# Optimization experiments

Measured on AMD Instinct MI355X. Metric: run time of the kernel, lower is better.

## Reference

```python
import jax, jax.numpy as jnp
import numpy as np

PARTIAL_DATA_THRESHOLD = 0.1  # threshold on squared NN distance (ChamferDistance returns squared dists)


def setup_inputs() -> dict:
    key = jax.random.key(0)
    k1, k2 = jax.random.split(key)
    scan_vertices = jax.random.normal(k1, (50000, 3), dtype=jnp.float32)      # N x 3
    template_vertices = jax.random.normal(k2, (6890, 3), dtype=jnp.float32)   # M x 3
    return {"scan_vertices": scan_vertices, "template_vertices": template_vertices}


def reference(scan_vertices, template_vertices):
    # Directional (template -> scan) Chamfer: for each template point, squared
    # distance to nearest scan point; then sum distances below threshold.
    # d2[m, n] = |t_m|^2 + |s_n|^2 - 2 t_m . s_n
    t_sq = jnp.sum(template_vertices * template_vertices, axis=-1)            # [M]
    s_sq = jnp.sum(scan_vertices * scan_vertices, axis=-1)                    # [N]
    cross = jnp.einsum('md,nd->mn', template_vertices, scan_vertices)         # [M, N]
    d2 = t_sq[:, None] + s_sq[None, :] - 2.0 * cross                          # [M, N]
    template2scan = jnp.min(d2, axis=1)                                       # [M]
    mask = template2scan < PARTIAL_DATA_THRESHOLD
    return jnp.sum(jnp.where(mask, template2scan, 0.0))
```

## Files before the change

### kernel.cpp

```cpp
#include <hip/hip_runtime.h>
#include <hip/hip_bf16.h>

#define BLK 256
#define SPLITS 44
#define FRTOT 1584
#define FPS (FRTOT / SPLITS)
#define NSLOT (FRTOT * 32)
#define THRESH 0.1f
#define KEY_MAX 0xFFFFFFFFu
#define ONE_BF ((unsigned short)0x3F80)

typedef __attribute__((ext_vector_type(8))) short short8;
typedef __attribute__((ext_vector_type(16))) float floatx16;

__device__ __forceinline__ unsigned short f2bf(float x) {
    unsigned u = __float_as_uint(x);
    unsigned r = u + 0x7FFFu + ((u >> 16) & 1u);
    return (unsigned short)(r >> 16);
}
__device__ __forceinline__ float bf2f(unsigned short h) {
    return __uint_as_float(((unsigned)h) << 16);
}

__device__ __forceinline__ unsigned f2key(float f) {
    unsigned b = __float_as_uint(f);
    return (b & 0x80000000u) ? ~b : (b | 0x80000000u);
}
__device__ __forceinline__ float key2f(unsigned k) {
    return __uint_as_float((k & 0x80000000u) ? (k & 0x7FFFFFFFu) : ~k);
}

template <int CTRL>
__device__ __forceinline__ float dpp_ror_min(float v) {
    const int i = __float_as_int(v);
    const int p = __builtin_amdgcn_update_dpp(i, i, CTRL, 0xF, 0xF, false);
    return fminf(v, __int_as_float(p));
}

__global__ __launch_bounds__(BLK) void pdl_prep(const float* __restrict__ scan,
                                                uint4* __restrict__ fragbuf,
                                                unsigned* __restrict__ gmin,
                                                float* __restrict__ out,
                                                int N, int Mpad) {
    const int n = blockIdx.x * BLK + threadIdx.x;
    if (n == 0) out[0] = 0.0f;
    if (n < Mpad) gmin[n] = KEY_MAX;
    if (n >= NSLOT) return;

    unsigned short k[16];
    if (n < N) {
        const float x = scan[3 * n + 0], y = scan[3 * n + 1], z = scan[3 * n + 2];
        const float s2 = fmaf(x, x, fmaf(y, y, z * z));
        const float cx = -2.0f * x, cy = -2.0f * y, cz = -2.0f * z;
        const unsigned short xh = f2bf(cx); const unsigned short xl = f2bf(cx - bf2f(xh));
        const unsigned short yh = f2bf(cy); const unsigned short yl = f2bf(cy - bf2f(yh));
        const unsigned short zh = f2bf(cz); const unsigned short zl = f2bf(cz - bf2f(zh));
        const unsigned short wh = f2bf(s2); const unsigned short wl = f2bf(s2 - bf2f(wh));
        k[0] = xh; k[1] = xl; k[2] = xh; k[3] = xl;
        k[4] = yh; k[5] = yl; k[6] = yh; k[7] = yl;
        k[8] = zh; k[9] = zl; k[10] = zh; k[11] = zl;
        k[12] = ONE_BF; k[13] = ONE_BF;
        k[14] = wh; k[15] = wl;
    } else {
#pragma unroll
        for (int i = 0; i < 16; ++i) k[i] = 0;
        k[12] = ONE_BF; k[13] = ONE_BF;
        k[14] = f2bf(1e30f); k[15] = 0;
    }

    const int g = n >> 5, c = n & 31;
    uint4 lo, hi;
    lo.x = (unsigned)k[0] | ((unsigned)k[1] << 16);
    lo.y = (unsigned)k[2] | ((unsigned)k[3] << 16);
    lo.z = (unsigned)k[4] | ((unsigned)k[5] << 16);
    lo.w = (unsigned)k[6] | ((unsigned)k[7] << 16);
    hi.x = (unsigned)k[8] | ((unsigned)k[9] << 16);
    hi.y = (unsigned)k[10] | ((unsigned)k[11] << 16);
    hi.z = (unsigned)k[12] | ((unsigned)k[13] << 16);
    hi.w = (unsigned)k[14] | ((unsigned)k[15] << 16);
    fragbuf[(size_t)g * 64 + c] = lo;
    fragbuf[(size_t)g * 64 + 32 + c] = hi;
}

__device__ __forceinline__ short8 make_A(const float* __restrict__ tmpl, int m, bool hi) {
    const float x = tmpl[3 * m + 0], y = tmpl[3 * m + 1], z = tmpl[3 * m + 2];
    const float t2 = fmaf(x, x, fmaf(y, y, z * z));
    const unsigned short xh = f2bf(x); const unsigned short xl = f2bf(x - bf2f(xh));
    const unsigned short yh = f2bf(y); const unsigned short yl = f2bf(y - bf2f(yh));
    const unsigned short zh = f2bf(z); const unsigned short zl = f2bf(z - bf2f(zh));
    const unsigned short wh = f2bf(t2); const unsigned short wl = f2bf(t2 - bf2f(wh));
    short8 A;
    A[0] = (short)(hi ? zh : xh);
    A[1] = (short)(hi ? zh : xh);
    A[2] = (short)(hi ? zl : xl);
    A[3] = (short)(hi ? zl : xl);
    A[4] = (short)(hi ? wh : yh);
    A[5] = (short)(hi ? wl : yh);
    A[6] = (short)(hi ? ONE_BF : yl);
    A[7] = (short)(hi ? ONE_BF : yl);
    return A;
}

__device__ __forceinline__ void reduce_store(floatx16 mn, int mbase, int lane,
                                             unsigned* __restrict__ gmin) {
#pragma unroll
    for (int r = 0; r < 16; ++r) {
        float v = mn[r];
        v = dpp_ror_min<0x128>(v);
        v = dpp_ror_min<0x124>(v);
        v = dpp_ror_min<0x122>(v);
        v = dpp_ror_min<0x121>(v);
        const int sw = __builtin_amdgcn_ds_swizzle(__float_as_int(v), 0x401F);
        v = fminf(v, __int_as_float(sw));
        if ((lane & 31) == 0) {
            const int row = (r & 3) + 8 * (r >> 2) + ((lane >> 5) << 2);
            atomicMin(&gmin[mbase + row], f2key(v));
        }
    }
}

__global__ __launch_bounds__(BLK, 4) void pdl_main(const float* __restrict__ tmpl,
                                                   const uint4* __restrict__ fragbuf,
                                                   unsigned* __restrict__ gmin,
                                                   int M) {
    const int tid = threadIdx.x;
    const int wave = tid >> 6, lane = tid & 63;
    const bool hi = (lane >= 32);

    const int mbase = (blockIdx.y * 4 + wave) * 64;
    int m0 = mbase + (lane & 31);       if (m0 > M - 1) m0 = M - 1;
    int m1 = mbase + 32 + (lane & 31);  if (m1 > M - 1) m1 = M - 1;
    const short8 A0 = make_A(tmpl, m0, hi);
    const short8 A1 = make_A(tmpl, m1, hi);

    floatx16 mn0, mn1, zacc;
#pragma unroll
    for (int r = 0; r < 16; ++r) { mn0[r] = 3e30f; mn1[r] = 3e30f; zacc[r] = 0.0f; }

    const uint4* fb = fragbuf + (size_t)(blockIdx.x * FPS) * 64 + lane;

    union U { uint4 u; short8 s; };
    uint4 p0 = fb[0];
    uint4 p1 = fb[64];
#pragma unroll 1
    for (int f = 0; f < FPS; f += 2) {
        U c0, c1; c0.u = p0; c1.u = p1;
        p0 = fb[(size_t)(f + 2) * 64];
        p1 = fb[(size_t)(f + 3) * 64];
        const floatx16 d00 = __builtin_amdgcn_mfma_f32_32x32x16_bf16(A0, c0.s, zacc, 0, 0, 0);
        const floatx16 d01 = __builtin_amdgcn_mfma_f32_32x32x16_bf16(A0, c1.s, zacc, 0, 0, 0);
#pragma unroll
        for (int r = 0; r < 16; ++r)
            mn0[r] = fminf(fminf(d00[r], d01[r]), mn0[r]);
        const floatx16 d10 = __builtin_amdgcn_mfma_f32_32x32x16_bf16(A1, c0.s, zacc, 0, 0, 0);
        const floatx16 d11 = __builtin_amdgcn_mfma_f32_32x32x16_bf16(A1, c1.s, zacc, 0, 0, 0);
#pragma unroll
        for (int r = 0; r < 16; ++r)
            mn1[r] = fminf(fminf(d10[r], d11[r]), mn1[r]);
    }

    reduce_store(mn0, mbase, lane, gmin);
    reduce_store(mn1, mbase + 32, lane, gmin);
}

__global__ __launch_bounds__(BLK) void pdl_final(const unsigned* __restrict__ gmin,
                                                 float* __restrict__ out, int M) {
    const int m = blockIdx.x * BLK + threadIdx.x;
    float s = 0.0f;
    if (m < M) {
        const float v = key2f(gmin[m]);
        if (v < THRESH) s = v;
    }
#pragma unroll
    for (int off = 32; off > 0; off >>= 1) s += __shfl_down(s, off, 64);

    __shared__ float ls[BLK / 64];
    const int lane = threadIdx.x & 63;
    const int w = threadIdx.x >> 6;
    if (lane == 0) ls[w] = s;
    __syncthreads();
    if (threadIdx.x == 0) {
        float t = 0.0f;
#pragma unroll
        for (int i = 0; i < BLK / 64; ++i) t += ls[i];
        atomicAdd(out, t);
    }
}

extern "C" void kernel_launch(void* const* d_in, const int* in_sizes, int n_in,
                              void* d_out, int out_size, void* d_ws, size_t ws_size,
                              hipStream_t stream) {
    const float* scan = (const float*)d_in[0];
    const float* tmpl = (const float*)d_in[1];
    float* out = (float*)d_out;

    const int N = in_sizes[0] / 3;
    const int M = in_sizes[1] / 3;

    const int tGroups = (M + 255) / 256;
    const int Mpad = ((M + 31) / 32) * 32 + 128;

    unsigned* gmin = (unsigned*)d_ws;
    uint4* fragbuf = (uint4*)((char*)d_ws + 65536);

    pdl_prep<<<(NSLOT + BLK - 1) / BLK, BLK, 0, stream>>>(scan, fragbuf, gmin,
                                                          out, N, Mpad);

    dim3 grid(SPLITS, tGroups);
    pdl_main<<<grid, BLK, 0, stream>>>(tmpl, fragbuf, gmin, M);

    pdl_final<<<(M + BLK - 1) / BLK, BLK, 0, stream>>>(gmin, out, M);
}
```

Measured before the change: 88.74 us.

## Give each wave four template tiles and split scan fragments across waves

The block's four waves now share one 128-row template block, and each wave walks a quarter of the block's scan-fragment range. Each scan fragment loaded is therefore reused across four template tiles instead of two. SPLITS is halved and the tGroups grid dimension doubles, so the total block count stays roughly the same. The change raises register pressure (four accumulator tiles, launch bounds lowered to 3) and doubles the atomicMin traffic per template row, because four waves now write the same rows.

```diff
diff --git a/kernel.cpp b/kernel.cpp
--- a/kernel.cpp
+++ b/kernel.cpp
@@ -2,9 +2,10 @@
 #include <hip/hip_bf16.h>
 
 #define BLK 256
-#define SPLITS 44
+#define SPLITS 22
 #define FRTOT 1584
 #define FPS (FRTOT / SPLITS)
+#define WFRAGS (FPS / 4)
 #define NSLOT (FRTOT * 32)
 #define THRESH 0.1f
 #define KEY_MAX 0xFFFFFFFFu
@@ -119,7 +120,7 @@
     }
 }
 
-__global__ __launch_bounds__(BLK, 4) void pdl_main(const float* __restrict__ tmpl,
+__global__ __launch_bounds__(BLK, 3) void pdl_main(const float* __restrict__ tmpl,
                                                    const uint4* __restrict__ fragbuf,
                                                    unsigned* __restrict__ gmin,
                                                    int M) {
@@ -127,40 +128,55 @@
     const int wave = tid >> 6, lane = tid & 63;
     const bool hi = (lane >= 32);
 
-    const int mbase = (blockIdx.y * 4 + wave) * 64;
-    int m0 = mbase + (lane & 31);       if (m0 > M - 1) m0 = M - 1;
-    int m1 = mbase + 32 + (lane & 31);  if (m1 > M - 1) m1 = M - 1;
+    const int mbase = blockIdx.y * 128;
+    int m0 = mbase + (lane & 31);        if (m0 > M - 1) m0 = M - 1;
+    int m1 = mbase + 32 + (lane & 31);   if (m1 > M - 1) m1 = M - 1;
+    int m2 = mbase + 64 + (lane & 31);   if (m2 > M - 1) m2 = M - 1;
+    int m3 = mbase + 96 + (lane & 31);   if (m3 > M - 1) m3 = M - 1;
     const short8 A0 = make_A(tmpl, m0, hi);
     const short8 A1 = make_A(tmpl, m1, hi);
-
-    floatx16 mn0, mn1, zacc;
-#pragma unroll
-    for (int r = 0; r < 16; ++r) { mn0[r] = 3e30f; mn1[r] = 3e30f; zacc[r] = 0.0f; }
-
-    const uint4* fb = fragbuf + (size_t)(blockIdx.x * FPS) * 64 + lane;
+    const short8 A2 = make_A(tmpl, m2, hi);
+    const short8 A3 = make_A(tmpl, m3, hi);
+
+    floatx16 mn0, mn1, mn2, mn3, zacc;
+#pragma unroll
+    for (int r = 0; r < 16; ++r) {
+        mn0[r] = 3e30f; mn1[r] = 3e30f; mn2[r] = 3e30f; mn3[r] = 3e30f;
+        zacc[r] = 0.0f;
+    }
+
+    const uint4* fb = fragbuf +
+        (size_t)(blockIdx.x * FPS + wave * WFRAGS) * 64 + lane;
 
     union U { uint4 u; short8 s; };
     uint4 p0 = fb[0];
     uint4 p1 = fb[64];
 #pragma unroll 1
-    for (int f = 0; f < FPS; f += 2) {
+    for (int f = 0; f < WFRAGS; f += 2) {
         U c0, c1; c0.u = p0; c1.u = p1;
         p0 = fb[(size_t)(f + 2) * 64];
         p1 = fb[(size_t)(f + 3) * 64];
-        const floatx16 d00 = __builtin_amdgcn_mfma_f32_32x32x16_bf16(A0, c0.s, zacc, 0, 0, 0);
-        const floatx16 d01 = __builtin_amdgcn_mfma_f32_32x32x16_bf16(A0, c1.s, zacc, 0, 0, 0);
-#pragma unroll
-        for (int r = 0; r < 16; ++r)
-            mn0[r] = fminf(fminf(d00[r], d01[r]), mn0[r]);
-        const floatx16 d10 = __builtin_amdgcn_mfma_f32_32x32x16_bf16(A1, c0.s, zacc, 0, 0, 0);
-        const floatx16 d11 = __builtin_amdgcn_mfma_f32_32x32x16_bf16(A1, c1.s, zacc, 0, 0, 0);
-#pragma unroll
-        for (int r = 0; r < 16; ++r)
-            mn1[r] = fminf(fminf(d10[r], d11[r]), mn1[r]);
+#define PDL_STEP(Af, mnf)                                                          \
+        {                                                                          \
+            const floatx16 d0 =                                                    \
+                __builtin_amdgcn_mfma_f32_32x32x16_bf16(Af, c0.s, zacc, 0, 0, 0);  \
+            const floatx16 d1 =                                                    \
+                __builtin_amdgcn_mfma_f32_32x32x16_bf16(Af, c1.s, zacc, 0, 0, 0);  \
+            _Pragma("unroll")                                                      \
+            for (int r = 0; r < 16; ++r)                                           \
+                mnf[r] = fminf(fminf(d0[r], d1[r]), mnf[r]);                       \
+        }
+        PDL_STEP(A0, mn0)
+        PDL_STEP(A1, mn1)
+        PDL_STEP(A2, mn2)
+        PDL_STEP(A3, mn3)
+#undef PDL_STEP
     }
 
     reduce_store(mn0, mbase, lane, gmin);
     reduce_store(mn1, mbase + 32, lane, gmin);
+    reduce_store(mn2, mbase + 64, lane, gmin);
+    reduce_store(mn3, mbase + 96, lane, gmin);
 }
 
 __global__ __launch_bounds__(BLK) void pdl_final(const unsigned* __restrict__ gmin,
@@ -197,7 +213,7 @@
     const int N = in_sizes[0] / 3;
     const int M = in_sizes[1] / 3;
 
-    const int tGroups = (M + 255) / 256;
+    const int tGroups = (M + 127) / 128;
     const int Mpad = ((M + 31) / 32) * 32 + 128;
 
     unsigned* gmin = (unsigned*)d_ws;
```

New measurement: 120.0 us. 35.2% more time.
